# Kernel tuning notes

Hardware: AMD Instinct MI355X
Metric: run time of the kernel (lower is better)

The kernel has to match this reference:

```python
import jax, jax.numpy as jnp
import numpy as np

B, H, W, DIM = 16, 64, 64, 256
EXPAND = 2
D_INNER = DIM * EXPAND      # 512
HID = D_INNER // 2          # 256 per GRU direction


def setup_inputs() -> dict:
    ks = jax.random.split(jax.random.key(0), 10)
    g = lambda i, shape, s=0.05: jax.random.normal(ks[i], shape, dtype=jnp.float32) * s
    return {
        "x": jax.random.normal(ks[0], (B, H, W, DIM), dtype=jnp.float32),
        "ln_gamma": jnp.ones((DIM,), jnp.float32),
        "ln_beta": jnp.zeros((DIM,), jnp.float32),
        "mlp_w1": g(1, (32, 4), 0.3),
        "mlp_b1": jnp.zeros((32,), jnp.float32),
        "mlp_w2": g(2, (4, 32), 0.3),
        "mlp_b2": jnp.zeros((4,), jnp.float32),
        "in_w": g(3, (D_INNER, DIM)),
        "in_b": jnp.zeros((D_INNER,), jnp.float32),
        "gru_wih_f": g(4, (3 * HID, D_INNER)),
        "gru_whh_f": g(5, (3 * HID, HID)),
        "gru_bih_f": jnp.zeros((3 * HID,), jnp.float32),
        "gru_bhh_f": jnp.zeros((3 * HID,), jnp.float32),
        "gru_wih_b": g(6, (3 * HID, D_INNER)),
        "gru_whh_b": g(7, (3 * HID, HID)),
        "gru_bih_b": jnp.zeros((3 * HID,), jnp.float32),
        "gru_bhh_b": jnp.zeros((3 * HID,), jnp.float32),
        "out_w": g(8, (DIM, D_INNER)),
        "out_b": jnp.zeros((DIM,), jnp.float32),
    }


def _resize_linear_axis(x, out_size, axis):
    """torch F.interpolate(mode='bilinear', align_corners=False) along one axis
    (the other axis has scale 1 -> identity, so 1-D resize is exact)."""
    in_size = x.shape[axis]
    scale = in_size / out_size
    src = (jnp.arange(out_size, dtype=jnp.float32) + 0.5) * scale - 0.5
    src = jnp.clip(src, 0.0, in_size - 1)
    i0 = jnp.floor(src).astype(jnp.int32)
    i1 = jnp.minimum(i0 + 1, in_size - 1)
    w = (src - i0.astype(jnp.float32))
    x0 = jnp.take(x, i0, axis=axis)
    x1 = jnp.take(x, i1, axis=axis)
    shape = [1] * x.ndim
    shape[axis] = out_size
    w = w.reshape(shape)
    return x0 * (1.0 - w) + x1 * w


def _avgpool3_mean(g):
    """F.avg_pool2d(g, 3, stride=1, padding=1) (count_include_pad=True), then
    spatial mean -> [B, 1]."""
    s = jax.lax.reduce_window(g, 0.0, jax.lax.add, (1, 1, 3, 3), (1, 1, 1, 1),
                              [(0, 0), (0, 0), (1, 1), (1, 1)])
    return (s / 9.0).mean(axis=(2, 3))


def _gru_dir(xp, whh, bhh, reverse):
    """One GRU direction. xp: [B, L, 3h] precomputed input-side gates."""
    hid = whh.shape[1]
    h0 = jnp.zeros((xp.shape[0], hid), xp.dtype)

    def step(h, xt):
        gh = h @ whh.T + bhh
        xr, xz, xn = jnp.split(xt, 3, axis=-1)
        hr, hz, hn = jnp.split(gh, 3, axis=-1)
        r = jax.nn.sigmoid(xr + hr)
        z = jax.nn.sigmoid(xz + hz)
        n = jnp.tanh(xn + r * hn)
        h_new = (1.0 - z) * n + z * h
        return h_new, h_new

    _, ys = jax.lax.scan(step, h0, jnp.swapaxes(xp, 0, 1), reverse=reverse)
    return jnp.swapaxes(ys, 0, 1)  # [B, L, h], ys[t] aligned with input t


def _forward(x, ln_gamma, ln_beta, mlp_w1, mlp_b1, mlp_w2, mlp_b2,
             in_w, in_b, gru_wih_f, gru_whh_f, gru_bih_f, gru_bhh_f,
             gru_wih_b, gru_whh_b, gru_bih_b, gru_bhh_b, out_w, out_b):
    Bx, Hx, Wx, C = x.shape
    # LayerNorm over channels
    mu = x.mean(-1, keepdims=True)
    var = ((x - mu) ** 2).mean(-1, keepdims=True)
    xn = (x - mu) / jnp.sqrt(var + 1e-5) * ln_gamma + ln_beta

    # --- GradientDirectionSelector ---
    gray = xn.mean(-1)[:, None]                                   # [B,1,H,W]
    gp = jnp.pad(gray, ((0, 0), (0, 0), (1, 1), (1, 1)), mode="reflect")
    grad_h = jnp.abs(gp[:, :, :, 2:] - gp[:, :, :, :-2])          # [B,1,H+2,W]
    grad_v = jnp.abs(gp[:, :, 2:, :] - gp[:, :, :-2, :])          # [B,1,H,W+2]
    grad_h = _resize_linear_axis(grad_h, Hx, axis=2)              # [B,1,H,W]
    grad_v = _resize_linear_axis(grad_v, Wx, axis=3)              # [B,1,H,W]
    grad_d = (grad_h + grad_v) * 0.5
    grad_a = jnp.abs(grad_h - grad_v)
    scores = jnp.concatenate(
        [_avgpool3_mean(g) for g in (grad_h, grad_v, grad_d, grad_a)], axis=1)  # [B,4]
    h1 = jax.nn.relu(scores @ mlp_w1.T + mlp_b1)
    logits = h1 @ mlp_w2.T + mlp_b2
    probs = jax.nn.softmax(logits, axis=-1)
    idx = jnp.argmax(probs, axis=-1)  # topk=1 indices, [B]

    # --- direction-routed scan (dir 1 -> vertical transpose; 0/2/3 -> row-major) ---
    seq_h = xn.reshape(Bx, Hx * Wx, C)
    seq_v = jnp.swapaxes(xn, 1, 2).reshape(Bx, Hx * Wx, C)
    seq = jnp.where((idx == 1)[:, None, None], seq_v, seq_h)      # [B,L,C]

    # --- FastSequenceBlock: in_proj -> biGRU -> out_proj ---
    z = seq @ in_w.T + in_b                                       # [B,L,d_inner]
    yf = _gru_dir(z @ gru_wih_f.T + gru_bih_f, gru_whh_f, gru_bhh_f, False)
    yb = _gru_dir(z @ gru_wih_b.T + gru_bih_b, gru_whh_b, gru_bhh_b, True)
    y = jnp.concatenate([yf, yb], axis=-1) @ out_w.T + out_b      # [B,L,C]

    # unscan (row-major reshape, as in the original) + residual
    return x + y.reshape(Bx, Hx, Wx, C)


def reference(x, ln_gamma, ln_beta, mlp_w1, mlp_b1, mlp_w2, mlp_b2,
              in_w, in_b, gru_wih_f, gru_whh_f, gru_bih_f, gru_bhh_f,
              gru_wih_b, gru_whh_b, gru_bih_b, gru_bhh_b, out_w, out_b):
    return _forward(x, ln_gamma, ln_beta, mlp_w1, mlp_b1, mlp_w2, mlp_b2,
                    in_w, in_b, gru_wih_f, gru_whh_f, gru_bih_f, gru_bhh_f,
                    gru_wih_b, gru_whh_b, gru_bih_b, gru_bhh_b, out_w, out_b)
```

## Files before the change

### kernel.cpp

```cpp
#include <hip/hip_runtime.h>


#define L_   4096
#define CH   32
#define NCH  128

typedef __attribute__((ext_vector_type(8))) _Float16 half8;
typedef __attribute__((ext_vector_type(4))) float f32x4;

__device__ __forceinline__ unsigned short f2h(float f) {
  _Float16 h = (_Float16)f;
  return __builtin_bit_cast(unsigned short, h);
}
__device__ __forceinline__ float h2f(unsigned short u) {
  return (float)__builtin_bit_cast(_Float16, u);
}
__device__ __forceinline__ float sigm(float x) {
  return __builtin_amdgcn_rcpf(1.f + __expf(-x));
}
__device__ __forceinline__ float tanhf_(float x) {
  return 1.f - 2.f * __builtin_amdgcn_rcpf(1.f + __expf(2.f * x));
}

__global__ __launch_bounds__(256) void k_f2h(const float* __restrict__ in,
                                             unsigned short* __restrict__ out,
                                             int n) {
  int i = blockIdx.x * 256 + threadIdx.x;
  if (i < n) out[i] = f2h(in[i]);
}

__global__ __launch_bounds__(256) void k_wcomb(const float* __restrict__ wih_f,
                                               const float* __restrict__ wih_b,
                                               const float* __restrict__ in_w,
                                               unsigned short* __restrict__ wcomb) {
  const int n = blockIdx.x;
  const float* wrow = (n < 768) ? (wih_f + (long)n * 512)
                                : (wih_b + (long)(n - 768) * 512);
  const int k = threadIdx.x;
  float acc = 0.f;
  for (int j = 0; j < 512; ++j) acc += wrow[j] * in_w[j * 256 + k];
  wcomb[(long)n * 256 + k] = f2h(acc);
}

__global__ __launch_bounds__(256) void k_bcomb(const float* __restrict__ wih_f,
                                               const float* __restrict__ wih_b,
                                               const float* __restrict__ in_b,
                                               const float* __restrict__ bih_f,
                                               const float* __restrict__ bih_b,
                                               const float* __restrict__ bhh_f,
                                               const float* __restrict__ bhh_b,
                                               float* __restrict__ badj) {
  int n = blockIdx.x * 256 + threadIdx.x;
  if (n >= 1536) return;
  const int dir = n >= 768;
  const int g = dir ? (n - 768) : n;
  const float* wrow = (dir ? wih_b : wih_f) + (long)g * 512;
  float acc = (dir ? bih_b : bih_f)[g];
  for (int j = 0; j < 512; ++j) acc += wrow[j] * in_b[j];
  if (g < 512) acc += (dir ? bhh_b : bhh_f)[g];
  badj[n] = acc;
}

__global__ __launch_bounds__(256) void k_ln(const float* __restrict__ x,
                                            const float* __restrict__ gamma,
                                            const float* __restrict__ beta,
                                            unsigned short* __restrict__ xn,
                                            float* __restrict__ gray) {
  const int lane = threadIdx.x & 63;
  const long pix = (long)blockIdx.x * 4 + (threadIdx.x >> 6);
  const float4 v = *(const float4*)(x + pix * 256 + lane * 4);
  float s = v.x + v.y + v.z + v.w;
  float s2 = v.x * v.x + v.y * v.y + v.z * v.z + v.w * v.w;
#pragma unroll
  for (int off = 32; off > 0; off >>= 1) {
    s += __shfl_xor(s, off, 64);
    s2 += __shfl_xor(s2, off, 64);
  }
  const float mu = s * (1.f / 256.f);
  const float var = fmaxf(s2 * (1.f / 256.f) - mu * mu, 0.f);
  const float rstd = rsqrtf(var + 1e-5f);
  const float4 gm = *(const float4*)(gamma + lane * 4);
  const float4 bt = *(const float4*)(beta + lane * 4);
  float o0 = (v.x - mu) * rstd * gm.x + bt.x;
  float o1 = (v.y - mu) * rstd * gm.y + bt.y;
  float o2 = (v.z - mu) * rstd * gm.z + bt.z;
  float o3 = (v.w - mu) * rstd * gm.w + bt.w;
  ushort4 o;
  o.x = f2h(o0); o.y = f2h(o1); o.z = f2h(o2); o.w = f2h(o3);
  *(ushort4*)(xn + pix * 256 + lane * 4) = o;
  float gs = o0 + o1 + o2 + o3;
#pragma unroll
  for (int off = 32; off > 0; off >>= 1) gs += __shfl_xor(gs, off, 64);
  if (lane == 0) gray[pix] = gs * (1.f / 256.f);
}

__device__ __forceinline__ int refl64(int m) {
  return m < 0 ? -m : (m > 63 ? 126 - m : m);
}

__global__ __launch_bounds__(256) void k_sel(const float* __restrict__ gray,
                                             const float* __restrict__ w1,
                                             const float* __restrict__ b1,
                                             const float* __restrict__ w2,
                                             const float* __restrict__ b2,
                                             int* __restrict__ flag) {
  __shared__ float g[64][65];
  __shared__ float part[4][4];
  const int b = blockIdx.x;
  const int tid = threadIdx.x;
  for (int r = 0; r < 16; ++r) {
    int p = tid + 256 * r;
    g[p >> 6][p & 63] = gray[(long)b * 4096 + p];
  }
  __syncthreads();
  const float S = 66.f / 64.f;
  float sh = 0.f, sv = 0.f, sd = 0.f, sa = 0.f;
  for (int rr = 0; rr < 16; ++rr) {
    int p = tid + 256 * rr;
    int h = p >> 6, w = p & 63;
    float srci = (h + 0.5f) * S - 0.5f;
    int i0 = (int)srci;
    float ai = srci - (float)i0;
    int i1 = i0 + 1; if (i1 > 65) i1 = 65;
    int r0 = refl64(i0 - 1), r1 = refl64(i1 - 1);
    int wl = w ? (w - 1) : 1;
    int wr2 = (w == 63) ? 62 : (w + 1);
    float GH0 = fabsf(g[r0][wr2] - g[r0][wl]);
    float GH1 = fabsf(g[r1][wr2] - g[r1][wl]);
    float ghr = GH0 + ai * (GH1 - GH0);
    float srcj = (w + 0.5f) * S - 0.5f;
    int j0 = (int)srcj;
    float aj = srcj - (float)j0;
    int j1 = j0 + 1; if (j1 > 65) j1 = 65;
    int c0 = refl64(j0 - 1), c1 = refl64(j1 - 1);
    int hu = h ? (h - 1) : 1;
    int hd = (h == 63) ? 62 : (h + 1);
    float GV0 = fabsf(g[hd][c0] - g[hu][c0]);
    float GV1 = fabsf(g[hd][c1] - g[hu][c1]);
    float gvr = GV0 + aj * (GV1 - GV0);
    float wt = ((h == 0 || h == 63) ? 2.f : 3.f) *
               ((w == 0 || w == 63) ? 2.f : 3.f);
    sh += wt * ghr;
    sv += wt * gvr;
    sd += wt * 0.5f * (ghr + gvr);
    sa += wt * fabsf(ghr - gvr);
  }
#pragma unroll
  for (int off = 32; off > 0; off >>= 1) {
    sh += __shfl_xor(sh, off, 64);
    sv += __shfl_xor(sv, off, 64);
    sd += __shfl_xor(sd, off, 64);
    sa += __shfl_xor(sa, off, 64);
  }
  if ((tid & 63) == 0) {
    part[tid >> 6][0] = sh; part[tid >> 6][1] = sv;
    part[tid >> 6][2] = sd; part[tid >> 6][3] = sa;
  }
  __syncthreads();
  if (tid == 0) {
    float sc[4];
    for (int k = 0; k < 4; ++k)
      sc[k] = (part[0][k] + part[1][k] + part[2][k] + part[3][k]) * (1.f / 36864.f);
    float logits[4];
    for (int k = 0; k < 4; ++k) logits[k] = b2[k];
    for (int j = 0; j < 32; ++j) {
      float hj = b1[j];
      for (int i = 0; i < 4; ++i) hj += sc[i] * w1[j * 4 + i];
      hj = fmaxf(hj, 0.f);
      for (int k = 0; k < 4; ++k) logits[k] += hj * w2[k * 32 + j];
    }
    int idx = 0;
    float best = logits[0];
    for (int k = 1; k < 4; ++k)
      if (logits[k] > best) { best = logits[k]; idx = k; }
    flag[b] = (idx == 1) ? 1 : 0;
  }
}

__global__ __launch_bounds__(256) void k_gemm(const unsigned short* __restrict__ A,
                                              const unsigned short* __restrict__ Bw,
                                              const float* __restrict__ bias,
                                              const float* __restrict__ resid,
                                              float* __restrict__ out,
                                              int K, int N) {
  __shared__ unsigned short Al[128][40];
  __shared__ unsigned short Bl[128][40];
  const int tid = threadIdx.x;
  const long m0 = (long)blockIdx.x * 128;
  const int n0 = blockIdx.y * 128;
  const int rA = tid >> 2;
  const int cp = (tid & 3) * 8;

  const unsigned short* a0p = A + (m0 + rA) * K + cp;
  const unsigned short* a1p = A + (m0 + rA + 64) * K + cp;
  const unsigned short* b0p = Bw + (long)(n0 + rA) * K + cp;
  const unsigned short* b1p = Bw + (long)(n0 + rA + 64) * K + cp;

  const int wv = tid >> 6, lane = tid & 63;
  const int wm = (wv >> 1) * 64, wn = (wv & 1) * 64;
  const int fr = lane & 15, fq = lane >> 4;

  const f32x4 zero4 = {0.f, 0.f, 0.f, 0.f};
  f32x4 acc[4][4];
#pragma unroll
  for (int i = 0; i < 4; ++i)
#pragma unroll
    for (int j = 0; j < 4; ++j) acc[i][j] = zero4;

  for (int k0 = 0; k0 < K; k0 += 32) {
    half8 va0 = *(const half8*)(a0p + k0);
    half8 va1 = *(const half8*)(a1p + k0);
    half8 vb0 = *(const half8*)(b0p + k0);
    half8 vb1 = *(const half8*)(b1p + k0);
    __syncthreads();
    *(half8*)&Al[rA][cp] = va0;
    *(half8*)&Al[rA + 64][cp] = va1;
    *(half8*)&Bl[rA][cp] = vb0;
    *(half8*)&Bl[rA + 64][cp] = vb1;
    __syncthreads();
    half8 af[4], bf[4];
#pragma unroll
    for (int i = 0; i < 4; ++i) af[i] = *(const half8*)&Al[wm + i * 16 + fr][fq * 8];
#pragma unroll
    for (int j = 0; j < 4; ++j) bf[j] = *(const half8*)&Bl[wn + j * 16 + fr][fq * 8];
#pragma unroll
    for (int i = 0; i < 4; ++i)
#pragma unroll
      for (int j = 0; j < 4; ++j)
        acc[i][j] = __builtin_amdgcn_mfma_f32_16x16x32_f16(af[i], bf[j], acc[i][j], 0, 0, 0);
  }

#pragma unroll
  for (int j = 0; j < 4; ++j) {
    const int col = n0 + wn + j * 16 + fr;
    const float bv = bias[col];
#pragma unroll
    for (int i = 0; i < 4; ++i) {
      const long mbase = m0 + wm + i * 16 + fq * 4;
#pragma unroll
      for (int r = 0; r < 4; ++r) {
        const long m = mbase + r;
        out[m * N + col] = acc[i][j][r] + bv + resid[m * N + col];
      }
    }
  }
}

__global__ __launch_bounds__(512, 2) void k_scan(
    const unsigned short* __restrict__ xn,
    const unsigned short* __restrict__ wcomb,
    const float* __restrict__ badj,
    const unsigned short* __restrict__ whh16,
    const float* __restrict__ bhhf,
    const float* __restrict__ bhhb,
    const int* __restrict__ flag,
    unsigned short* __restrict__ ycat) {
  const int dir = blockIdx.x & 1;
  const int b = blockIdx.x >> 1;
  const unsigned short* whh = whh16 + (long)dir * (768 * 256);
  const float* bhh = dir ? bhhb : bhhf;
  const unsigned short* wcd = wcomb + (long)dir * (768 * 256);
  const float* bcd = badj + dir * 768;
  const int tid = threadIdx.x;
  const int wv = tid >> 6;
  const int lane = tid & 63;
  const int fr = lane & 15;
  const int fq = lane >> 4;
  const int fb = flag[b];

  half8 wf[6][8];
#pragma unroll
  for (int j = 0; j < 6; ++j) {
    const int n = (j >> 1) * 256 + wv * 32 + (j & 1) * 16 + fr;
    const unsigned short* wrow = whh + (long)n * 256 + fq * 8;
#pragma unroll
    for (int s = 0; s < 8; ++s) wf[j][s] = *(const half8*)(wrow + s * 32);
  }
#pragma unroll
  for (int j = 0; j < 6; ++j)
#pragma unroll
    for (int s = 0; s < 8; ++s) asm volatile("" : "+v"(wf[j][s]));

  __shared__ unsigned short xplds[CH][768];
  __shared__ unsigned short ylds[CH][256];
  __shared__ unsigned short hbuf[2][272];

  const int u0 = wv * 32 + fr;
  float Bnh0 = 0.f, Bnh1 = 0.f, h0 = 0.f, h1 = 0.f;
  if (lane < 16) {
    Bnh0 = bhh[512 + u0];
    Bnh1 = bhh[512 + u0 + 16];
  }
  if (tid < 272) hbuf[0][tid] = 0;
  if (tid < 16) hbuf[1][256 + tid] = 0;
  __syncthreads();

  const long xnb = (long)b * 4096;
  unsigned short* yb = ycat + (long)b * (L_ * 512) + dir * 256;

  const f32x4 zero4 = {0.f, 0.f, 0.f, 0.f};
  int pb = 0;

  for (int c = 0; c < NCH; ++c) {
    const int cc = dir ? (NCH - 1 - c) : c;
    const int t0 = cc * CH;

    if (c > 0) {
      const int pt0 = (dir ? (NCH - c) : (c - 1)) * CH;
#pragma unroll
      for (int k = 0; k < 2; ++k) {
        const int idx = tid * 2 + k;
        const int ts = idx >> 5;
        const int cl = (idx & 31) * 8;
        half8 v = *(const half8*)&ylds[ts][cl];
        *(half8*)(yb + (long)(pt0 + ts) * 512 + cl) = v;
      }
    }

    const unsigned short* arow0;
    const unsigned short* arow1;
    {
      int t = t0 + fr;
      int p = fb ? (((t & 63) << 6) | (t >> 6)) : t;
      arow0 = xn + (xnb + p) * 256 + fq * 8;
      t = t0 + 16 + fr;
      p = fb ? (((t & 63) << 6) | (t >> 6)) : t;
      arow1 = xn + (xnb + p) * 256 + fq * 8;
    }
#pragma unroll
    for (int hf = 0; hf < 2; ++hf) {
      f32x4 acc0[3], acc1[3];
#pragma unroll
      for (int i = 0; i < 3; ++i) { acc0[i] = zero4; acc1[i] = zero4; }
#pragma unroll
      for (int s = 0; s < 8; ++s) {
        half8 a0 = *(const half8*)(arow0 + s * 32);
        half8 a1 = *(const half8*)(arow1 + s * 32);
#pragma unroll
        for (int i = 0; i < 3; ++i) {
          const int jj = hf * 3 + i;
          const int n = (jj >> 1) * 256 + wv * 32 + (jj & 1) * 16 + fr;
          half8 bfr = *(const half8*)(wcd + (long)n * 256 + s * 32 + fq * 8);
          acc0[i] = __builtin_amdgcn_mfma_f32_16x16x32_f16(a0, bfr, acc0[i], 0, 0, 0);
          acc1[i] = __builtin_amdgcn_mfma_f32_16x16x32_f16(a1, bfr, acc1[i], 0, 0, 0);
        }
      }
#pragma unroll
      for (int i = 0; i < 3; ++i) {
        const int jj = hf * 3 + i;
        const int n = (jj >> 1) * 256 + wv * 32 + (jj & 1) * 16 + fr;
        const float bv = bcd[n];
#pragma unroll
        for (int r = 0; r < 4; ++r) {
          xplds[fq * 4 + r][n] = f2h(acc0[i][r] + bv);
          xplds[16 + fq * 4 + r][n] = f2h(acc1[i][r] + bv);
        }
      }
    }
    __syncthreads();

    for (int lt = 0; lt < CH; ++lt) {
      const int ts = dir ? (CH - 1 - lt) : lt;
      float xr0 = 0.f, xr1 = 0.f, xz0 = 0.f, xz1 = 0.f, xn0 = 0.f, xn1 = 0.f;
      if (lane < 16) {
        xr0 = h2f(xplds[ts][u0]);
        xr1 = h2f(xplds[ts][u0 + 16]);
        xz0 = h2f(xplds[ts][256 + u0]);
        xz1 = h2f(xplds[ts][256 + u0 + 16]);
        xn0 = h2f(xplds[ts][512 + u0]);
        xn1 = h2f(xplds[ts][512 + u0 + 16]);
      }
      f32x4 acc[6];
#pragma unroll
      for (int j = 0; j < 6; ++j) acc[j] = zero4;
#pragma unroll
      for (int s = 0; s < 8; ++s) {
        const half8 a =
            *(const half8*)&hbuf[pb][(fr == 0) ? (s * 32 + fq * 8) : 256];
#pragma unroll
        for (int j = 0; j < 6; ++j)
          acc[j] = __builtin_amdgcn_mfma_f32_16x16x32_f16(a, wf[j][s], acc[j], 0, 0, 0);
      }
      if (lane < 16) {
        float r0 = sigm(xr0 + acc[0][0]);
        float r1 = sigm(xr1 + acc[1][0]);
        float z0 = sigm(xz0 + acc[2][0]);
        float z1 = sigm(xz1 + acc[3][0]);
        float n0 = tanhf_(xn0 + r0 * (acc[4][0] + Bnh0));
        float n1 = tanhf_(xn1 + r1 * (acc[5][0] + Bnh1));
        h0 = n0 + z0 * (h0 - n0);
        h1 = n1 + z1 * (h1 - n1);
        unsigned short hb0 = f2h(h0);
        unsigned short hb1 = f2h(h1);
        hbuf[pb ^ 1][u0] = hb0;
        hbuf[pb ^ 1][u0 + 16] = hb1;
        ylds[ts][u0] = hb0;
        ylds[ts][u0 + 16] = hb1;
      }
      pb ^= 1;
      __syncthreads();
    }
  }
  {
    const int pt0 = (dir ? 0 : (NCH - 1)) * CH;
#pragma unroll
    for (int k = 0; k < 2; ++k) {
      const int idx = tid * 2 + k;
      const int ts = idx >> 5;
      const int cl = (idx & 31) * 8;
      half8 v = *(const half8*)&ylds[ts][cl];
      *(half8*)(yb + (long)(pt0 + ts) * 512 + cl) = v;
    }
  }
}

extern "C" void kernel_launch(void* const* d_in, const int* in_sizes, int n_in,
                              void* d_out, int out_size, void* d_ws, size_t ws_size,
                              hipStream_t stream) {
  (void)in_sizes; (void)n_in; (void)out_size; (void)ws_size;
  const float* x     = (const float*)d_in[0];
  const float* lng   = (const float*)d_in[1];
  const float* lnb   = (const float*)d_in[2];
  const float* w1    = (const float*)d_in[3];
  const float* b1    = (const float*)d_in[4];
  const float* w2    = (const float*)d_in[5];
  const float* b2    = (const float*)d_in[6];
  const float* in_w  = (const float*)d_in[7];
  const float* in_b  = (const float*)d_in[8];
  const float* wih_f = (const float*)d_in[9];
  const float* whh_f = (const float*)d_in[10];
  const float* bih_f = (const float*)d_in[11];
  const float* bhh_f = (const float*)d_in[12];
  const float* wih_b = (const float*)d_in[13];
  const float* whh_b = (const float*)d_in[14];
  const float* bih_b = (const float*)d_in[15];
  const float* bhh_b = (const float*)d_in[16];
  const float* out_w = (const float*)d_in[17];
  const float* out_b = (const float*)d_in[18];

  char* ws = (char*)d_ws;
  unsigned short* xn     = (unsigned short*)(ws + 0);
  float*          gray   = (float*)(ws + 33554432);
  int*            flag   = (int*)(ws + 33816576);
  unsigned short* whh16  = (unsigned short*)(ws + 33816832);
  unsigned short* outw16 = (unsigned short*)(ws + 34603264);
  unsigned short* wcomb  = (unsigned short*)(ws + 34865408);
  float*          badj   = (float*)(ws + 35651840);
  unsigned short* ycat   = (unsigned short*)(ws + 35658240);

  k_f2h<<<768, 256, 0, stream>>>(whh_f, whh16, 196608);
  k_f2h<<<768, 256, 0, stream>>>(whh_b, whh16 + 196608, 196608);
  k_f2h<<<512, 256, 0, stream>>>(out_w, outw16, 131072);
  k_wcomb<<<1536, 256, 0, stream>>>(wih_f, wih_b, in_w, wcomb);
  k_bcomb<<<6, 256, 0, stream>>>(wih_f, wih_b, in_b, bih_f, bih_b,
                                 bhh_f, bhh_b, badj);
  k_ln<<<16384, 256, 0, stream>>>(x, lng, lnb, xn, gray);
  k_sel<<<16, 256, 0, stream>>>(gray, w1, b1, w2, b2, flag);
  k_scan<<<32, 512, 0, stream>>>(xn, wcomb, badj, whh16,
                                 bhh_f, bhh_b, flag, ycat);
  dim3 gout(512, 2);
  k_gemm<<<gout, 256, 0, stream>>>(ycat, outw16, out_b, x, (float*)d_out, 512, 256);
}
```

Baseline: 6.988 ms.

## Replace MFMA recurrent matvec with per-thread fdot2 rows across 768 threads

The GRU scan kernel now uses 768 threads, one per gate row. Each thread computes its hidden-state dot product with packed fp16 dot2 instructions against a broadcast h vector in LDS, replacing 16x16 MFMAs that wasted 15 of 16 rows on a single-vector matvec. Gate pre-activations are exchanged through a small LDS buffer with an extra barrier per step. The input projection is re-tiled to 4 column tiles per wave. The recurrent weights (32 uint4 per thread) are reloaded from global memory at the start of every chunk rather than held for the whole kernel, which adds memory traffic and register pressure.

```diff
diff --git a/kernel.cpp b/kernel.cpp
--- a/kernel.cpp
+++ b/kernel.cpp
@@ -6,6 +6,7 @@
 #define NCH  128
 
 typedef __attribute__((ext_vector_type(8))) _Float16 half8;
+typedef __attribute__((ext_vector_type(2))) _Float16 half2v;
 typedef __attribute__((ext_vector_type(4))) float f32x4;
 
 __device__ __forceinline__ unsigned short f2h(float f) {
@@ -20,6 +21,10 @@
 }
 __device__ __forceinline__ float tanhf_(float x) {
   return 1.f - 2.f * __builtin_amdgcn_rcpf(1.f + __expf(2.f * x));
+}
+__device__ __forceinline__ float dot2(unsigned w, unsigned h, float c) {
+  return __builtin_amdgcn_fdot2(__builtin_bit_cast(half2v, w),
+                                __builtin_bit_cast(half2v, h), c, false);
 }
 
 __global__ __launch_bounds__(256) void k_f2h(const float* __restrict__ in,
@@ -246,7 +251,7 @@
   }
 }
 
-__global__ __launch_bounds__(512, 2) void k_scan(
+__global__ __launch_bounds__(768, 3) void k_scan(
     const unsigned short* __restrict__ xn,
     const unsigned short* __restrict__ wcomb,
     const float* __restrict__ badj,
@@ -262,38 +267,23 @@
   const unsigned short* wcd = wcomb + (long)dir * (768 * 256);
   const float* bcd = badj + dir * 768;
   const int tid = threadIdx.x;
+  const int g = tid >> 8;
+  const int u = tid & 255;
   const int wv = tid >> 6;
   const int lane = tid & 63;
   const int fr = lane & 15;
   const int fq = lane >> 4;
   const int fb = flag[b];
 
-  half8 wf[6][8];
-#pragma unroll
-  for (int j = 0; j < 6; ++j) {
-    const int n = (j >> 1) * 256 + wv * 32 + (j & 1) * 16 + fr;
-    const unsigned short* wrow = whh + (long)n * 256 + fq * 8;
-#pragma unroll
-    for (int s = 0; s < 8; ++s) wf[j][s] = *(const half8*)(wrow + s * 32);
-  }
-#pragma unroll
-  for (int j = 0; j < 6; ++j)
-#pragma unroll
-    for (int s = 0; s < 8; ++s) asm volatile("" : "+v"(wf[j][s]));
-
   __shared__ unsigned short xplds[CH][768];
   __shared__ unsigned short ylds[CH][256];
-  __shared__ unsigned short hbuf[2][272];
-
-  const int u0 = wv * 32 + fr;
-  float Bnh0 = 0.f, Bnh1 = 0.f, h0 = 0.f, h1 = 0.f;
-  if (lane < 16) {
-    Bnh0 = bhh[512 + u0];
-    Bnh1 = bhh[512 + u0 + 16];
-  }
-  if (tid < 272) hbuf[0][tid] = 0;
-  if (tid < 16) hbuf[1][256 + tid] = 0;
-  __syncthreads();
+  __shared__ uint4 hl4[2][32];
+  __shared__ float ghlds[512];
+
+  float Bnh = 0.f;
+  if (g == 2) Bnh = bhh[512 + u];
+  float hreg = 0.f;
+  if (tid < 128) ((unsigned*)hl4[0])[tid] = 0;
 
   const long xnb = (long)b * 4096;
   unsigned short* yb = ycat + (long)b * (L_ * 512) + dir * 256;
@@ -309,46 +299,45 @@
       const int pt0 = (dir ? (NCH - c) : (c - 1)) * CH;
 #pragma unroll
       for (int k = 0; k < 2; ++k) {
-        const int idx = tid * 2 + k;
-        const int ts = idx >> 5;
-        const int cl = (idx & 31) * 8;
-        half8 v = *(const half8*)&ylds[ts][cl];
-        *(half8*)(yb + (long)(pt0 + ts) * 512 + cl) = v;
-      }
-    }
-
-    const unsigned short* arow0;
-    const unsigned short* arow1;
+        const int idx = tid + 768 * k;
+        if (idx < 1024) {
+          const int tsx = idx >> 5;
+          const int cl = (idx & 31) * 8;
+          half8 v = *(const half8*)&ylds[tsx][cl];
+          *(half8*)(yb + (long)(pt0 + tsx) * 512 + cl) = v;
+        }
+      }
+    }
+
     {
-      int t = t0 + fr;
-      int p = fb ? (((t & 63) << 6) | (t >> 6)) : t;
-      arow0 = xn + (xnb + p) * 256 + fq * 8;
-      t = t0 + 16 + fr;
-      p = fb ? (((t & 63) << 6) | (t >> 6)) : t;
-      arow1 = xn + (xnb + p) * 256 + fq * 8;
-    }
-#pragma unroll
-    for (int hf = 0; hf < 2; ++hf) {
-      f32x4 acc0[3], acc1[3];
-#pragma unroll
-      for (int i = 0; i < 3; ++i) { acc0[i] = zero4; acc1[i] = zero4; }
+      const unsigned short* arow0;
+      const unsigned short* arow1;
+      {
+        int t = t0 + fr;
+        int p = fb ? (((t & 63) << 6) | (t >> 6)) : t;
+        arow0 = xn + (xnb + p) * 256 + fq * 8;
+        t = t0 + 16 + fr;
+        p = fb ? (((t & 63) << 6) | (t >> 6)) : t;
+        arow1 = xn + (xnb + p) * 256 + fq * 8;
+      }
+      f32x4 acc0[4], acc1[4];
+#pragma unroll
+      for (int i = 0; i < 4; ++i) { acc0[i] = zero4; acc1[i] = zero4; }
 #pragma unroll
       for (int s = 0; s < 8; ++s) {
-        half8 a0 = *(const half8*)(arow0 + s * 32);
-        half8 a1 = *(const half8*)(arow1 + s * 32);
-#pragma unroll
-        for (int i = 0; i < 3; ++i) {
-          const int jj = hf * 3 + i;
-          const int n = (jj >> 1) * 256 + wv * 32 + (jj & 1) * 16 + fr;
+        half8 a0v = *(const half8*)(arow0 + s * 32);
+        half8 a1v = *(const half8*)(arow1 + s * 32);
+#pragma unroll
+        for (int i = 0; i < 4; ++i) {
+          const int n = (wv * 4 + i) * 16 + fr;
           half8 bfr = *(const half8*)(wcd + (long)n * 256 + s * 32 + fq * 8);
-          acc0[i] = __builtin_amdgcn_mfma_f32_16x16x32_f16(a0, bfr, acc0[i], 0, 0, 0);
-          acc1[i] = __builtin_amdgcn_mfma_f32_16x16x32_f16(a1, bfr, acc1[i], 0, 0, 0);
+          acc0[i] = __builtin_amdgcn_mfma_f32_16x16x32_f16(a0v, bfr, acc0[i], 0, 0, 0);
+          acc1[i] = __builtin_amdgcn_mfma_f32_16x16x32_f16(a1v, bfr, acc1[i], 0, 0, 0);
         }
       }
 #pragma unroll
-      for (int i = 0; i < 3; ++i) {
-        const int jj = hf * 3 + i;
-        const int n = (jj >> 1) * 256 + wv * 32 + (jj & 1) * 16 + fr;
+      for (int i = 0; i < 4; ++i) {
+        const int n = (wv * 4 + i) * 16 + fr;
         const float bv = bcd[n];
 #pragma unroll
         for (int r = 0; r < 4; ++r) {
@@ -359,43 +348,38 @@
     }
     __syncthreads();
 
+    uint4 wq[32];
+    {
+      const unsigned short* wp = whh + (long)tid * 256;
+      asm volatile("" : "+v"(wp));
+#pragma unroll
+      for (int i = 0; i < 32; ++i) wq[i] = *(const uint4*)(wp + i * 8);
+    }
+
     for (int lt = 0; lt < CH; ++lt) {
       const int ts = dir ? (CH - 1 - lt) : lt;
-      float xr0 = 0.f, xr1 = 0.f, xz0 = 0.f, xz1 = 0.f, xn0 = 0.f, xn1 = 0.f;
-      if (lane < 16) {
-        xr0 = h2f(xplds[ts][u0]);
-        xr1 = h2f(xplds[ts][u0 + 16]);
-        xz0 = h2f(xplds[ts][256 + u0]);
-        xz1 = h2f(xplds[ts][256 + u0 + 16]);
-        xn0 = h2f(xplds[ts][512 + u0]);
-        xn1 = h2f(xplds[ts][512 + u0 + 16]);
-      }
-      f32x4 acc[6];
-#pragma unroll
-      for (int j = 0; j < 6; ++j) acc[j] = zero4;
-#pragma unroll
-      for (int s = 0; s < 8; ++s) {
-        const half8 a =
-            *(const half8*)&hbuf[pb][(fr == 0) ? (s * 32 + fq * 8) : 256];
-#pragma unroll
-        for (int j = 0; j < 6; ++j)
-          acc[j] = __builtin_amdgcn_mfma_f32_16x16x32_f16(a, wf[j][s], acc[j], 0, 0, 0);
-      }
-      if (lane < 16) {
-        float r0 = sigm(xr0 + acc[0][0]);
-        float r1 = sigm(xr1 + acc[1][0]);
-        float z0 = sigm(xz0 + acc[2][0]);
-        float z1 = sigm(xz1 + acc[3][0]);
-        float n0 = tanhf_(xn0 + r0 * (acc[4][0] + Bnh0));
-        float n1 = tanhf_(xn1 + r1 * (acc[5][0] + Bnh1));
-        h0 = n0 + z0 * (h0 - n0);
-        h1 = n1 + z1 * (h1 - n1);
-        unsigned short hb0 = f2h(h0);
-        unsigned short hb1 = f2h(h1);
-        hbuf[pb ^ 1][u0] = hb0;
-        hbuf[pb ^ 1][u0 + 16] = hb1;
-        ylds[ts][u0] = hb0;
-        ylds[ts][u0 + 16] = hb1;
+      const uint4* hp = hl4[pb];
+      float a0 = 0.f, a1 = 0.f, a2 = 0.f, a3 = 0.f;
+#pragma unroll
+      for (int i = 0; i < 32; ++i) {
+        uint4 hv = hp[i];
+        a0 = dot2(wq[i].x, hv.x, a0);
+        a1 = dot2(wq[i].y, hv.y, a1);
+        a2 = dot2(wq[i].z, hv.z, a2);
+        a3 = dot2(wq[i].w, hv.w, a3);
+      }
+      const float gh = (a0 + a1) + (a2 + a3);
+      if (g == 1) ghlds[u] = h2f(xplds[ts][tid]) + gh;
+      else if (g == 2) ghlds[256 + u] = gh + Bnh;
+      __syncthreads();
+      if (g == 0) {
+        const float r = sigm(h2f(xplds[ts][u]) + gh);
+        const float z = sigm(ghlds[u]);
+        const float n = tanhf_(h2f(xplds[ts][512 + u]) + r * ghlds[256 + u]);
+        hreg = n + z * (hreg - n);
+        const unsigned short hb = f2h(hreg);
+        ((unsigned short*)hl4[pb ^ 1])[u] = hb;
+        ylds[ts][u] = hb;
       }
       pb ^= 1;
       __syncthreads();
@@ -405,11 +389,13 @@
     const int pt0 = (dir ? 0 : (NCH - 1)) * CH;
 #pragma unroll
     for (int k = 0; k < 2; ++k) {
-      const int idx = tid * 2 + k;
-      const int ts = idx >> 5;
-      const int cl = (idx & 31) * 8;
-      half8 v = *(const half8*)&ylds[ts][cl];
-      *(half8*)(yb + (long)(pt0 + ts) * 512 + cl) = v;
+      const int idx = tid + 768 * k;
+      if (idx < 1024) {
+        const int tsx = idx >> 5;
+        const int cl = (idx & 31) * 8;
+        half8 v = *(const half8*)&ylds[tsx][cl];
+        *(half8*)(yb + (long)(pt0 + tsx) * 512 + cl) = v;
+      }
     }
   }
 }
@@ -456,7 +442,7 @@
                                  bhh_f, bhh_b, badj);
   k_ln<<<16384, 256, 0, stream>>>(x, lng, lnb, xn, gray);
   k_sel<<<16, 256, 0, stream>>>(gray, w1, b1, w2, b2, flag);
-  k_scan<<<32, 512, 0, stream>>>(xn, wcomb, badj, whh16,
+  k_scan<<<32, 768, 0, stream>>>(xn, wcomb, badj, whh16,
                                  bhh_f, bhh_b, flag, ycat);
   dim3 gout(512, 2);
   k_gemm<<<gout, 256, 0, stream>>>(ycat, outw16, out_b, x, (float*)d_out, 512, 256);
```

New measurement: 8.337 ms. 1.19x slower.
